# Kernel optimization log

Measured on AMD Instinct MI355X. Metric: run time of the kernel, lower is better.

The kernel has to match this reference:

```python
import jax, jax.numpy as jnp
import numpy as np

IN_C = 256
OUT_C = 256
HID = IN_C * 2
N_POINTS = 262144
N_NODES = 8192
B = 16
MAX_NODES = 512
EPS = 1e-5


def _mlp(h, w1, b1, g1, be1, w2, b2):
    # PyG MLP([C, 2C, out], norm='layer_norm'): lin -> layernorm -> relu -> (dropout, eval=identity) -> lin
    h = h @ w1 + b1
    mu = jnp.mean(h, axis=-1, keepdims=True)
    var = jnp.var(h, axis=-1, keepdims=True)
    h = (h - mu) * jax.lax.rsqrt(var + EPS) * g1 + be1
    h = jax.nn.relu(h)
    return h @ w2 + b2


def setup_inputs() -> dict:
    key = jax.random.key(0)
    ks = jax.random.split(key, 16)
    x = jax.random.normal(ks[0], (N_POINTS, IN_C), dtype=jnp.float32)
    f_point_batches = jnp.sort(jax.random.randint(ks[1], (N_POINTS,), 0, N_NODES)).astype(jnp.int32)
    # equal-sized graphs (16 graphs x 512 nodes), sorted as torch.split/pad_sequence assume
    g_node_batches = jnp.repeat(jnp.arange(B, dtype=jnp.int32), MAX_NODES)
    s = 1.0 / np.sqrt(IN_C)
    s2 = 1.0 / np.sqrt(HID)
    def lin(k, fan_in, shape, scale):
        return jax.random.uniform(k, shape, jnp.float32, -scale, scale)
    params = {}
    for i, name in enumerate(['Wq', 'Wk']):
        base = 2 + i * 6
        params[f'{name}_w1'] = lin(ks[base + 0], IN_C, (IN_C, HID), s)
        params[f'{name}_b1'] = lin(ks[base + 1], IN_C, (HID,), s)
        params[f'{name}_g1'] = jnp.ones((HID,), jnp.float32)
        params[f'{name}_be1'] = jnp.zeros((HID,), jnp.float32)
        params[f'{name}_w2'] = lin(ks[base + 2], HID, (HID, OUT_C), s2)
        params[f'{name}_b2'] = lin(ks[base + 3], HID, (OUT_C,), s2)
    return dict(x=x, f_point_batches=f_point_batches, g_node_batches=g_node_batches,
                num_graphs=B, max_nodes=MAX_NODES, **params)


def reference(x, f_point_batches, g_node_batches, num_graphs, max_nodes,
              Wq_w1, Wq_b1, Wq_g1, Wq_be1, Wq_w2, Wq_b2,
              Wk_w1, Wk_b1, Wk_g1, Wk_be1, Wk_w2, Wk_b2):
    n_nodes = g_node_batches.shape[0]
    C = x.shape[1]
    # scatter_mean over points -> per-node feature means [n_nodes, C]
    sums = jax.ops.segment_sum(x, f_point_batches, num_segments=n_nodes)
    cnt = jax.ops.segment_sum(jnp.ones((x.shape[0],), x.dtype), f_point_batches, num_segments=n_nodes)
    mean = sums / jnp.maximum(cnt, 1.0)[:, None]
    # ragged split by graph + pad_sequence -> [B, max_nodes, C]
    starts = jnp.searchsorted(g_node_batches, jnp.arange(num_graphs, dtype=g_node_batches.dtype))
    pos = jnp.arange(n_nodes) - starts[g_node_batches]
    padded = jnp.zeros((num_graphs, max_nodes, C), x.dtype).at[g_node_batches, pos].set(mean, mode='drop')
    q = _mlp(padded, Wq_w1, Wq_b1, Wq_g1, Wq_be1, Wq_w2, Wq_b2)  # [B, MAXN, out]
    k = _mlp(padded, Wk_w1, Wk_b1, Wk_g1, Wk_be1, Wk_w2, Wk_b2)
    return jnp.einsum('bnd,bmd->bnm', q, k)  # bmm(q, k^T)
```

## Files before the change

### kernel.cpp

```cpp
#include <hip/hip_runtime.h>
#include <hip/hip_bf16.h>

#define N_POINTS 262144
#define N_NODES  8192
#define IN_C     256
#define HID      512
#define OUT_C    256
#define NB       16
#define MAXN     512
#define EPSV     1e-5f

typedef __attribute__((ext_vector_type(8))) short short8;
typedef __attribute__((ext_vector_type(4))) float f32x4;
#define MFMA16(a, b, c) __builtin_amdgcn_mfma_f32_16x16x32_bf16((a), (b), (c), 0, 0, 0)


__global__ __launch_bounds__(256) void prelude_k(
    const int* __restrict__ fpb, int* __restrict__ starts,
    const float* __restrict__ W1q, const float* __restrict__ W1k,
    const float* __restrict__ W2q, const float* __restrict__ W2k,
    __hip_bfloat16* __restrict__ P1q, __hip_bfloat16* __restrict__ P1k,
    __hip_bfloat16* __restrict__ P2q, __hip_bfloat16* __restrict__ P2k)
{
  if (blockIdx.x < 1024) {
    const int i = blockIdx.x * 256 + threadIdx.x;
    const int cur = fpb[i];
    const int prev = (i == 0) ? -1 : fpb[i - 1];
    for (int n = prev + 1; n <= cur; ++n) starts[n] = i;
    if (i == N_POINTS - 1)
      for (int n = cur + 1; n <= N_NODES; ++n) starts[n] = N_POINTS;
    return;
  }
  const int bid = blockIdx.x - 1024;
  const int sel = bid >> 6;
  const float* W; __hip_bfloat16* P; int N;
  switch (sel) {
    case 0:  W = W1q; P = P1q; N = HID;   break;
    case 1:  W = W1k; P = P1k; N = HID;   break;
    case 2:  W = W2q; P = P2q; N = OUT_C; break;
    default: W = W2k; P = P2k; N = OUT_C; break;
  }
  const int idx = (bid & 63) * 256 + threadIdx.x;
  const int NF = N >> 4;
  const int lane = idx & 63;
  const int nf = (idx >> 6) % NF;
  const int ks = idx / (64 * NF);
  const int k0 = ks * 32 + (lane >> 4) * 8;
  const int n  = nf * 16 + (lane & 15);
  __hip_bfloat16 tmp[8];
  #pragma unroll
  for (int j = 0; j < 8; ++j) tmp[j] = __float2bfloat16(W[(size_t)(k0 + j) * N + n]);
  *(uint4*)(P + (size_t)idx * 8) = *(uint4*)tmp;
}

__global__ __launch_bounds__(256) void scatter_mean_k(
    const float* __restrict__ x, const int* __restrict__ starts,
    __hip_bfloat16* __restrict__ mean)
{
  const int node = blockIdx.x;
  const int start = starts[node];
  const int end   = starts[node + 1];
  const int t  = threadIdx.x;
  const int c4 = t & 63;
  const int rr = t >> 6;

  float4 s = make_float4(0.f, 0.f, 0.f, 0.f);
  for (int r = start + rr; r < end; r += 4) {
    float4 v = *(const float4*)(x + (size_t)r * IN_C + c4 * 4);
    s.x += v.x; s.y += v.y; s.z += v.z; s.w += v.w;
  }

  __shared__ float4 red[256];
  red[t] = s;
  __syncthreads();
  if (t < 64) {
    float4 a = red[t], b = red[t + 64], c = red[t + 128], d = red[t + 192];
    const int cnt = end - start;
    const float inv = cnt > 0 ? 1.0f / (float)cnt : 0.0f;
    __hip_bfloat16 o[4];
    o[0] = __float2bfloat16((a.x + b.x + c.x + d.x) * inv);
    o[1] = __float2bfloat16((a.y + b.y + c.y + d.y) * inv);
    o[2] = __float2bfloat16((a.z + b.z + c.z + d.z) * inv);
    o[3] = __float2bfloat16((a.w + b.w + c.w + d.w) * inv);
    *(uint2*)(mean + (size_t)node * IN_C + t * 4) = *(uint2*)o;
  }
}

__global__ __launch_bounds__(256, 2) void mlp_fused_k(
    const __hip_bfloat16* __restrict__ mean,
    const __hip_bfloat16* __restrict__ P1q, const __hip_bfloat16* __restrict__ P2q,
    const float* __restrict__ b1q, const float* __restrict__ g1q,
    const float* __restrict__ be1q, const float* __restrict__ b2q,
    const __hip_bfloat16* __restrict__ P1k, const __hip_bfloat16* __restrict__ P2k,
    const float* __restrict__ b1k, const float* __restrict__ g1k,
    const float* __restrict__ be1k, const float* __restrict__ b2k,
    __hip_bfloat16* __restrict__ qo, __hip_bfloat16* __restrict__ ko)
{
  const int head = blockIdx.y;
  const __hip_bfloat16* P1 = head ? P1k : P1q;
  const __hip_bfloat16* P2 = head ? P2k : P2q;
  const float* b1  = head ? b1k  : b1q;
  const float* g1  = head ? g1k  : g1q;
  const float* be1 = head ? be1k : be1q;
  const float* b2  = head ? b2k  : b2q;
  __hip_bfloat16* out = head ? ko : qo;

  const int row0 = blockIdx.x * 64;
  const int t = threadIdx.x;
  const int w  = t >> 6;
  const int l  = t & 63;
  const int lg = l >> 4;
  const int lm = l & 15;

  __shared__ __hip_bfloat16 HsRaw[64 * 520];
  __shared__ float lnp[4][64][2];
  __hip_bfloat16* As = HsRaw;

  #pragma unroll
  for (int it = 0; it < 8; ++it) {
    const int idx = t + it * 256;
    const int r = idx >> 5, c8 = idx & 31;
    uint4 v = *(const uint4*)(mean + (size_t)(row0 + r) * IN_C + c8 * 8);
    *(uint4*)(As + r * 264 + c8 * 8) = v;
  }
  __syncthreads();

  f32x4 acc1[4][8];
  #pragma unroll
  for (int mi = 0; mi < 4; ++mi)
    #pragma unroll
    for (int nj = 0; nj < 8; ++nj)
      #pragma unroll
      for (int r = 0; r < 4; ++r) acc1[mi][nj][r] = 0.f;

  for (int ks = 0; ks < 8; ++ks) {
    short8 a[4], b[8];
    #pragma unroll
    for (int mi = 0; mi < 4; ++mi)
      a[mi] = *(const short8*)(As + (mi * 16 + lm) * 264 + ks * 32 + lg * 8);
    const __hip_bfloat16* bp = P1 + ((size_t)(ks * 32 + w * 8) * 64 + l) * 8;
    #pragma unroll
    for (int nj = 0; nj < 8; ++nj)
      b[nj] = *(const short8*)(bp + (size_t)nj * 64 * 8);
    #pragma unroll
    for (int mi = 0; mi < 4; ++mi)
      #pragma unroll
      for (int nj = 0; nj < 8; ++nj)
        acc1[mi][nj] = MFMA16(a[mi], b[nj], acc1[mi][nj]);
  }

  float b1v[8], g1v[8], e1v[8];
  #pragma unroll
  for (int nj = 0; nj < 8; ++nj) {
    const int c = w * 128 + nj * 16 + lm;
    b1v[nj] = b1[c]; g1v[nj] = g1[c]; e1v[nj] = be1[c];
  }
  #pragma unroll
  for (int mi = 0; mi < 4; ++mi)
    #pragma unroll
    for (int nj = 0; nj < 8; ++nj)
      #pragma unroll
      for (int r = 0; r < 4; ++r) acc1[mi][nj][r] += b1v[nj];

  float sums[4][4], sqs[4][4];
  #pragma unroll
  for (int mi = 0; mi < 4; ++mi)
    #pragma unroll
    for (int r = 0; r < 4; ++r) {
      float s = 0.f, q = 0.f;
      #pragma unroll
      for (int nj = 0; nj < 8; ++nj) {
        const float xv = acc1[mi][nj][r];
        s += xv; q += xv * xv;
      }
      #pragma unroll
      for (int off = 1; off < 16; off <<= 1) {
        s += __shfl_xor(s, off);
        q += __shfl_xor(q, off);
      }
      sums[mi][r] = s; sqs[mi][r] = q;
    }
  if (lm == 0) {
    #pragma unroll
    for (int mi = 0; mi < 4; ++mi)
      #pragma unroll
      for (int r = 0; r < 4; ++r) {
        const int row = mi * 16 + lg * 4 + r;
        lnp[w][row][0] = sums[mi][r];
        lnp[w][row][1] = sqs[mi][r];
      }
  }
  __syncthreads();

  #pragma unroll
  for (int mi = 0; mi < 4; ++mi) {
    #pragma unroll
    for (int r = 0; r < 4; ++r) {
      const int row = mi * 16 + lg * 4 + r;
      float S = 0.f, Q = 0.f;
      #pragma unroll
      for (int w2 = 0; w2 < 4; ++w2) { S += lnp[w2][row][0]; Q += lnp[w2][row][1]; }
      const float mu = S * (1.0f / HID);
      const float var = Q * (1.0f / HID) - mu * mu;
      const float rs = rsqrtf(var + EPSV);
      #pragma unroll
      for (int nj = 0; nj < 8; ++nj) {
        const float y = (acc1[mi][nj][r] - mu) * rs * g1v[nj] + e1v[nj];
        HsRaw[row * 520 + w * 128 + nj * 16 + lm] = __float2bfloat16(fmaxf(y, 0.f));
      }
    }
  }
  __syncthreads();

  f32x4 acc2[4][4];
  #pragma unroll
  for (int mi = 0; mi < 4; ++mi)
    #pragma unroll
    for (int nj = 0; nj < 4; ++nj)
      #pragma unroll
      for (int r = 0; r < 4; ++r) acc2[mi][nj][r] = 0.f;

  for (int ks = 0; ks < 16; ++ks) {
    short8 a2[4], b2f[4];
    #pragma unroll
    for (int mi = 0; mi < 4; ++mi)
      a2[mi] = *(const short8*)(HsRaw + (mi * 16 + lm) * 520 + ks * 32 + lg * 8);
    const __hip_bfloat16* bp2 = P2 + ((size_t)(ks * 16 + w * 4) * 64 + l) * 8;
    #pragma unroll
    for (int nj = 0; nj < 4; ++nj)
      b2f[nj] = *(const short8*)(bp2 + (size_t)nj * 64 * 8);
    #pragma unroll
    for (int mi = 0; mi < 4; ++mi)
      #pragma unroll
      for (int nj = 0; nj < 4; ++nj)
        acc2[mi][nj] = MFMA16(a2[mi], b2f[nj], acc2[mi][nj]);
  }

  float b2v[4];
  #pragma unroll
  for (int nj = 0; nj < 4; ++nj) b2v[nj] = b2[w * 64 + nj * 16 + lm];
  #pragma unroll
  for (int mi = 0; mi < 4; ++mi)
    #pragma unroll
    for (int nj = 0; nj < 4; ++nj)
      #pragma unroll
      for (int r = 0; r < 4; ++r) {
        const int row = row0 + mi * 16 + lg * 4 + r;
        const int col = w * 64 + nj * 16 + lm;
        out[(size_t)row * OUT_C + col] = __float2bfloat16(acc2[mi][nj][r] + b2v[nj]);
      }
}

__global__ __launch_bounds__(256) void bmm_k(
    const __hip_bfloat16* __restrict__ q, const __hip_bfloat16* __restrict__ k,
    float* __restrict__ out)
{
  const int b  = blockIdx.z;
  const int n0 = blockIdx.x * 128;
  const int m0 = blockIdx.y * 128;
  const int t = threadIdx.x;
  const int w = t >> 6, l = t & 63, lg = l >> 4, lm = l & 15;
  const int wm = w >> 1, wn = w & 1;

  const __hip_bfloat16* qb = q + ((size_t)b * MAXN + n0 + wm * 64) * OUT_C;
  const __hip_bfloat16* kb = k + ((size_t)b * MAXN + m0 + wn * 64) * OUT_C;

  f32x4 acc[4][4];
  #pragma unroll
  for (int mi = 0; mi < 4; ++mi)
    #pragma unroll
    for (int nj = 0; nj < 4; ++nj)
      #pragma unroll
      for (int r = 0; r < 4; ++r) acc[mi][nj][r] = 0.f;

  for (int ks = 0; ks < 8; ++ks) {
    short8 a[4], bb[4];
    #pragma unroll
    for (int mi = 0; mi < 4; ++mi)
      a[mi] = *(const short8*)(qb + (size_t)(mi * 16 + lm) * OUT_C + ks * 32 + lg * 8);
    #pragma unroll
    for (int nj = 0; nj < 4; ++nj)
      bb[nj] = *(const short8*)(kb + (size_t)(nj * 16 + lm) * OUT_C + ks * 32 + lg * 8);
    #pragma unroll
    for (int mi = 0; mi < 4; ++mi)
      #pragma unroll
      for (int nj = 0; nj < 4; ++nj)
        acc[mi][nj] = MFMA16(a[mi], bb[nj], acc[mi][nj]);
  }

  #pragma unroll
  for (int mi = 0; mi < 4; ++mi)
    #pragma unroll
    for (int nj = 0; nj < 4; ++nj)
      #pragma unroll
      for (int r = 0; r < 4; ++r) {
        const int nrow = n0 + wm * 64 + mi * 16 + lg * 4 + r;
        const int mcol = m0 + wn * 64 + nj * 16 + lm;
        out[((size_t)b * MAXN + nrow) * MAXN + mcol] = acc[mi][nj][r];
      }
}

extern "C" void kernel_launch(void* const* d_in, const int* in_sizes, int n_in,
                              void* d_out, int out_size, void* d_ws, size_t ws_size,
                              hipStream_t stream)
{
  const float* x   = (const float*)d_in[0];
  const int*   fpb = (const int*)d_in[1];
  const float* Wq_w1  = (const float*)d_in[5];
  const float* Wq_b1  = (const float*)d_in[6];
  const float* Wq_g1  = (const float*)d_in[7];
  const float* Wq_be1 = (const float*)d_in[8];
  const float* Wq_w2  = (const float*)d_in[9];
  const float* Wq_b2  = (const float*)d_in[10];
  const float* Wk_w1  = (const float*)d_in[11];
  const float* Wk_b1  = (const float*)d_in[12];
  const float* Wk_g1  = (const float*)d_in[13];
  const float* Wk_be1 = (const float*)d_in[14];
  const float* Wk_w2  = (const float*)d_in[15];
  const float* Wk_b2  = (const float*)d_in[16];

  __hip_bfloat16* ws = (__hip_bfloat16*)d_ws;
  __hip_bfloat16* P1q  = ws;
  __hip_bfloat16* P1k  = P1q + 131072;
  __hip_bfloat16* P2q  = P1k + 131072;
  __hip_bfloat16* P2k  = P2q + 131072;
  __hip_bfloat16* mean = P2k + 131072;
  __hip_bfloat16* qo   = mean + 2097152;
  __hip_bfloat16* ko   = qo + 2097152;
  int* starts = (int*)(ko + 2097152);
  float* out = (float*)d_out;

  prelude_k<<<1280, 256, 0, stream>>>(fpb, starts,
      Wq_w1, Wk_w1, Wq_w2, Wk_w2, P1q, P1k, P2q, P2k);
  scatter_mean_k<<<N_NODES, 256, 0, stream>>>(x, starts, mean);
  mlp_fused_k<<<dim3(N_NODES / 64, 2), 256, 0, stream>>>(
      mean, P1q, P2q, Wq_b1, Wq_g1, Wq_be1, Wq_b2,
      P1k, P2k, Wk_b1, Wk_g1, Wk_be1, Wk_b2, qo, ko);
  bmm_k<<<dim3(4, 4, NB), 256, 0, stream>>>(qo, ko, out);
}
```

Before: 102.0 us.

## Retile MLP and BMM kernels for more blocks and add dual accumulators in scatter

The scatter-mean loop now keeps two independent accumulators so more loads are in flight at once. The fused MLP kernel computes both heads in one 512-thread block over 32 rows, giving 256 blocks instead of 256 two-head blocks of 64 rows, and each block stages the shared input only once. The BMM kernel switches to 64x64 tiles (1024 blocks) to fill more compute units. In exchange, each block reuses the weight fragments over fewer rows, so more weight traffic goes to L2.

```diff
diff --git a/kernel.cpp b/kernel.cpp
--- a/kernel.cpp
+++ b/kernel.cpp
@@ -9,6 +9,7 @@
 #define NB       16
 #define MAXN     512
 #define EPSV     1e-5f
+#define NPB      32
 
 typedef __attribute__((ext_vector_type(8))) short short8;
 typedef __attribute__((ext_vector_type(4))) float f32x4;
@@ -64,14 +65,23 @@
   const int c4 = t & 63;
   const int rr = t >> 6;
 
-  float4 s = make_float4(0.f, 0.f, 0.f, 0.f);
-  for (int r = start + rr; r < end; r += 4) {
+  float4 s0 = make_float4(0.f, 0.f, 0.f, 0.f);
+  float4 s1 = make_float4(0.f, 0.f, 0.f, 0.f);
+  int r = start + rr;
+  for (; r + 8 <= end; r += 8) {
+    float4 v0 = *(const float4*)(x + (size_t)r * IN_C + c4 * 4);
+    float4 v1 = *(const float4*)(x + (size_t)(r + 4) * IN_C + c4 * 4);
+    s0.x += v0.x; s0.y += v0.y; s0.z += v0.z; s0.w += v0.w;
+    s1.x += v1.x; s1.y += v1.y; s1.z += v1.z; s1.w += v1.w;
+  }
+  for (; r < end; r += 4) {
     float4 v = *(const float4*)(x + (size_t)r * IN_C + c4 * 4);
-    s.x += v.x; s.y += v.y; s.z += v.z; s.w += v.w;
-  }
+    s0.x += v.x; s0.y += v.y; s0.z += v.z; s0.w += v.w;
+  }
+  s0.x += s1.x; s0.y += s1.y; s0.z += s1.z; s0.w += s1.w;
 
   __shared__ float4 red[256];
-  red[t] = s;
+  red[t] = s0;
   __syncthreads();
   if (t < 64) {
     float4 a = red[t], b = red[t + 64], c = red[t + 128], d = red[t + 192];
@@ -86,7 +96,7 @@
   }
 }
 
-__global__ __launch_bounds__(256, 2) void mlp_fused_k(
+__global__ __launch_bounds__(512, 2) void mlp_fused_k(
     const __hip_bfloat16* __restrict__ mean,
     const __hip_bfloat16* __restrict__ P1q, const __hip_bfloat16* __restrict__ P2q,
     const float* __restrict__ b1q, const float* __restrict__ g1q,
@@ -96,208 +106,181 @@
     const float* __restrict__ be1k, const float* __restrict__ b2k,
     __hip_bfloat16* __restrict__ qo, __hip_bfloat16* __restrict__ ko)
 {
-  const int head = blockIdx.y;
-  const __hip_bfloat16* P1 = head ? P1k : P1q;
-  const __hip_bfloat16* P2 = head ? P2k : P2q;
-  const float* b1  = head ? b1k  : b1q;
-  const float* g1  = head ? g1k  : g1q;
-  const float* be1 = head ? be1k : be1q;
-  const float* b2  = head ? b2k  : b2q;
-  __hip_bfloat16* out = head ? ko : qo;
-
-  const int row0 = blockIdx.x * 64;
+  const int n0 = blockIdx.x * NPB;
   const int t = threadIdx.x;
-  const int w  = t >> 6;
-  const int l  = t & 63;
-  const int lg = l >> 4;
-  const int lm = l & 15;
-
-  __shared__ __hip_bfloat16 HsRaw[64 * 520];
-  __shared__ float lnp[4][64][2];
-  __hip_bfloat16* As = HsRaw;
-
-  #pragma unroll
-  for (int it = 0; it < 8; ++it) {
-    const int idx = t + it * 256;
+  const int w = t >> 6, l = t & 63, lg = l >> 4, lm = l & 15;
+  const int h = w >> 2;
+  const int c = w & 3;
+
+  const __hip_bfloat16* P1 = h ? P1k : P1q;
+  const __hip_bfloat16* P2 = h ? P2k : P2q;
+  const float* b1  = h ? b1k  : b1q;
+  const float* g1  = h ? g1k  : g1q;
+  const float* be1 = h ? be1k : be1q;
+  const float* b2  = h ? b2k  : b2q;
+  __hip_bfloat16* out = h ? ko : qo;
+
+  __shared__ __hip_bfloat16 As[NPB * 264];
+  __shared__ __hip_bfloat16 Hs[2][NPB * 520];
+  __shared__ float lnp[8][NPB][2];
+
+  #pragma unroll
+  for (int it = 0; it < 2; ++it) {
+    const int idx = t + it * 512;
     const int r = idx >> 5, c8 = idx & 31;
-    uint4 v = *(const uint4*)(mean + (size_t)(row0 + r) * IN_C + c8 * 8);
+    uint4 v = *(const uint4*)(mean + (size_t)(n0 + r) * IN_C + c8 * 8);
     *(uint4*)(As + r * 264 + c8 * 8) = v;
   }
   __syncthreads();
 
-  f32x4 acc1[4][8];
-  #pragma unroll
-  for (int mi = 0; mi < 4; ++mi)
+  f32x4 acc1[2][8];
+  #pragma unroll
+  for (int mi = 0; mi < 2; ++mi)
     #pragma unroll
     for (int nj = 0; nj < 8; ++nj)
       #pragma unroll
       for (int r = 0; r < 4; ++r) acc1[mi][nj][r] = 0.f;
 
   for (int ks = 0; ks < 8; ++ks) {
-    short8 a[4], b[8];
-    #pragma unroll
-    for (int mi = 0; mi < 4; ++mi)
-      a[mi] = *(const short8*)(As + (mi * 16 + lm) * 264 + ks * 32 + lg * 8);
-    const __hip_bfloat16* bp = P1 + ((size_t)(ks * 32 + w * 8) * 64 + l) * 8;
+    short8 a0 = *(const short8*)(As + lm * 264 + ks * 32 + lg * 8);
+    short8 a1 = *(const short8*)(As + (16 + lm) * 264 + ks * 32 + lg * 8);
+    const __hip_bfloat16* bp = P1 + ((size_t)(ks * 32 + c * 8) * 64 + l) * 8;
+    #pragma unroll
+    for (int nj = 0; nj < 8; ++nj) {
+      short8 b = *(const short8*)(bp + (size_t)nj * 512);
+      acc1[0][nj] = MFMA16(a0, b, acc1[0][nj]);
+      acc1[1][nj] = MFMA16(a1, b, acc1[1][nj]);
+    }
+  }
+
+  float b1v[8], g1v[8], e1v[8];
+  #pragma unroll
+  for (int nj = 0; nj < 8; ++nj) {
+    const int col = c * 128 + nj * 16 + lm;
+    b1v[nj] = b1[col]; g1v[nj] = g1[col]; e1v[nj] = be1[col];
+  }
+  #pragma unroll
+  for (int mi = 0; mi < 2; ++mi)
     #pragma unroll
     for (int nj = 0; nj < 8; ++nj)
-      b[nj] = *(const short8*)(bp + (size_t)nj * 64 * 8);
-    #pragma unroll
-    for (int mi = 0; mi < 4; ++mi)
-      #pragma unroll
-      for (int nj = 0; nj < 8; ++nj)
-        acc1[mi][nj] = MFMA16(a[mi], b[nj], acc1[mi][nj]);
-  }
-
-  float b1v[8], g1v[8], e1v[8];
-  #pragma unroll
-  for (int nj = 0; nj < 8; ++nj) {
-    const int c = w * 128 + nj * 16 + lm;
-    b1v[nj] = b1[c]; g1v[nj] = g1[c]; e1v[nj] = be1[c];
-  }
-  #pragma unroll
-  for (int mi = 0; mi < 4; ++mi)
-    #pragma unroll
-    for (int nj = 0; nj < 8; ++nj)
       #pragma unroll
       for (int r = 0; r < 4; ++r) acc1[mi][nj][r] += b1v[nj];
 
-  float sums[4][4], sqs[4][4];
-  #pragma unroll
-  for (int mi = 0; mi < 4; ++mi)
+  #pragma unroll
+  for (int mi = 0; mi < 2; ++mi)
     #pragma unroll
     for (int r = 0; r < 4; ++r) {
       float s = 0.f, q = 0.f;
       #pragma unroll
       for (int nj = 0; nj < 8; ++nj) {
-        const float xv = acc1[mi][nj][r];
-        s += xv; q += xv * xv;
+        const float v = acc1[mi][nj][r];
+        s += v; q += v * v;
       }
       #pragma unroll
       for (int off = 1; off < 16; off <<= 1) {
         s += __shfl_xor(s, off);
         q += __shfl_xor(q, off);
       }
-      sums[mi][r] = s; sqs[mi][r] = q;
-    }
-  if (lm == 0) {
-    #pragma unroll
-    for (int mi = 0; mi < 4; ++mi)
-      #pragma unroll
-      for (int r = 0; r < 4; ++r) {
+      if (lm == 0) {
         const int row = mi * 16 + lg * 4 + r;
-        lnp[w][row][0] = sums[mi][r];
-        lnp[w][row][1] = sqs[mi][r];
-      }
-  }
+        lnp[w][row][0] = s;
+        lnp[w][row][1] = q;
+      }
+    }
   __syncthreads();
 
   #pragma unroll
-  for (int mi = 0; mi < 4; ++mi) {
+  for (int mi = 0; mi < 2; ++mi)
     #pragma unroll
     for (int r = 0; r < 4; ++r) {
       const int row = mi * 16 + lg * 4 + r;
       float S = 0.f, Q = 0.f;
       #pragma unroll
-      for (int w2 = 0; w2 < 4; ++w2) { S += lnp[w2][row][0]; Q += lnp[w2][row][1]; }
+      for (int w2 = 0; w2 < 4; ++w2) {
+        S += lnp[h * 4 + w2][row][0];
+        Q += lnp[h * 4 + w2][row][1];
+      }
       const float mu = S * (1.0f / HID);
-      const float var = Q * (1.0f / HID) - mu * mu;
-      const float rs = rsqrtf(var + EPSV);
+      const float rs = rsqrtf(Q * (1.0f / HID) - mu * mu + EPSV);
       #pragma unroll
       for (int nj = 0; nj < 8; ++nj) {
         const float y = (acc1[mi][nj][r] - mu) * rs * g1v[nj] + e1v[nj];
-        HsRaw[row * 520 + w * 128 + nj * 16 + lm] = __float2bfloat16(fmaxf(y, 0.f));
-      }
-    }
-  }
+        Hs[h][row * 520 + c * 128 + nj * 16 + lm] = __float2bfloat16(fmaxf(y, 0.f));
+      }
+    }
   __syncthreads();
 
-  f32x4 acc2[4][4];
-  #pragma unroll
-  for (int mi = 0; mi < 4; ++mi)
+  f32x4 acc2[2][4];
+  #pragma unroll
+  for (int mi = 0; mi < 2; ++mi)
     #pragma unroll
     for (int nj = 0; nj < 4; ++nj)
       #pragma unroll
       for (int r = 0; r < 4; ++r) acc2[mi][nj][r] = 0.f;
 
   for (int ks = 0; ks < 16; ++ks) {
-    short8 a2[4], b2f[4];
-    #pragma unroll
-    for (int mi = 0; mi < 4; ++mi)
-      a2[mi] = *(const short8*)(HsRaw + (mi * 16 + lm) * 520 + ks * 32 + lg * 8);
-    const __hip_bfloat16* bp2 = P2 + ((size_t)(ks * 16 + w * 4) * 64 + l) * 8;
+    short8 a0 = *(const short8*)(Hs[h] + lm * 520 + ks * 32 + lg * 8);
+    short8 a1 = *(const short8*)(Hs[h] + (16 + lm) * 520 + ks * 32 + lg * 8);
+    const __hip_bfloat16* bp = P2 + ((size_t)(ks * 16 + c * 4) * 64 + l) * 8;
+    #pragma unroll
+    for (int nj = 0; nj < 4; ++nj) {
+      short8 b = *(const short8*)(bp + (size_t)nj * 512);
+      acc2[0][nj] = MFMA16(a0, b, acc2[0][nj]);
+      acc2[1][nj] = MFMA16(a1, b, acc2[1][nj]);
+    }
+  }
+
+  float b2v[4];
+  #pragma unroll
+  for (int nj = 0; nj < 4; ++nj) b2v[nj] = b2[c * 64 + nj * 16 + lm];
+  #pragma unroll
+  for (int mi = 0; mi < 2; ++mi)
     #pragma unroll
     for (int nj = 0; nj < 4; ++nj)
-      b2f[nj] = *(const short8*)(bp2 + (size_t)nj * 64 * 8);
-    #pragma unroll
-    for (int mi = 0; mi < 4; ++mi)
-      #pragma unroll
-      for (int nj = 0; nj < 4; ++nj)
-        acc2[mi][nj] = MFMA16(a2[mi], b2f[nj], acc2[mi][nj]);
-  }
-
-  float b2v[4];
-  #pragma unroll
-  for (int nj = 0; nj < 4; ++nj) b2v[nj] = b2[w * 64 + nj * 16 + lm];
-  #pragma unroll
-  for (int mi = 0; mi < 4; ++mi)
-    #pragma unroll
-    for (int nj = 0; nj < 4; ++nj)
       #pragma unroll
       for (int r = 0; r < 4; ++r) {
-        const int row = row0 + mi * 16 + lg * 4 + r;
-        const int col = w * 64 + nj * 16 + lm;
+        const int row = n0 + mi * 16 + lg * 4 + r;
+        const int col = c * 64 + nj * 16 + lm;
         out[(size_t)row * OUT_C + col] = __float2bfloat16(acc2[mi][nj][r] + b2v[nj]);
       }
 }
 
-__global__ __launch_bounds__(256) void bmm_k(
+__global__ __launch_bounds__(256, 4) void bmm_k(
     const __hip_bfloat16* __restrict__ q, const __hip_bfloat16* __restrict__ k,
     float* __restrict__ out)
 {
   const int b  = blockIdx.z;
-  const int n0 = blockIdx.x * 128;
-  const int m0 = blockIdx.y * 128;
+  const int n0 = blockIdx.x * 64;
+  const int m0 = blockIdx.y * 64;
   const int t = threadIdx.x;
   const int w = t >> 6, l = t & 63, lg = l >> 4, lm = l & 15;
-  const int wm = w >> 1, wn = w & 1;
-
-  const __hip_bfloat16* qb = q + ((size_t)b * MAXN + n0 + wm * 64) * OUT_C;
-  const __hip_bfloat16* kb = k + ((size_t)b * MAXN + m0 + wn * 64) * OUT_C;
-
-  f32x4 acc[4][4];
-  #pragma unroll
-  for (int mi = 0; mi < 4; ++mi)
-    #pragma unroll
-    for (int nj = 0; nj < 4; ++nj)
-      #pragma unroll
-      for (int r = 0; r < 4; ++r) acc[mi][nj][r] = 0.f;
+
+  const __hip_bfloat16* qb = q + ((size_t)b * MAXN + n0 + w * 16) * OUT_C;
+  const __hip_bfloat16* kb = k + ((size_t)b * MAXN + m0) * OUT_C;
+
+  f32x4 acc[4];
+  #pragma unroll
+  for (int nj = 0; nj < 4; ++nj)
+    #pragma unroll
+    for (int r = 0; r < 4; ++r) acc[nj][r] = 0.f;
 
   for (int ks = 0; ks < 8; ++ks) {
-    short8 a[4], bb[4];
-    #pragma unroll
-    for (int mi = 0; mi < 4; ++mi)
-      a[mi] = *(const short8*)(qb + (size_t)(mi * 16 + lm) * OUT_C + ks * 32 + lg * 8);
-    #pragma unroll
-    for (int nj = 0; nj < 4; ++nj)
-      bb[nj] = *(const short8*)(kb + (size_t)(nj * 16 + lm) * OUT_C + ks * 32 + lg * 8);
-    #pragma unroll
-    for (int mi = 0; mi < 4; ++mi)
-      #pragma unroll
-      for (int nj = 0; nj < 4; ++nj)
-        acc[mi][nj] = MFMA16(a[mi], bb[nj], acc[mi][nj]);
-  }
-
-  #pragma unroll
-  for (int mi = 0; mi < 4; ++mi)
-    #pragma unroll
-    for (int nj = 0; nj < 4; ++nj)
-      #pragma unroll
-      for (int r = 0; r < 4; ++r) {
-        const int nrow = n0 + wm * 64 + mi * 16 + lg * 4 + r;
-        const int mcol = m0 + wn * 64 + nj * 16 + lm;
-        out[((size_t)b * MAXN + nrow) * MAXN + mcol] = acc[mi][nj][r];
-      }
+    short8 a = *(const short8*)(qb + (size_t)lm * OUT_C + ks * 32 + lg * 8);
+    #pragma unroll
+    for (int nj = 0; nj < 4; ++nj) {
+      short8 bb = *(const short8*)(kb + (size_t)(nj * 16 + lm) * OUT_C + ks * 32 + lg * 8);
+      acc[nj] = MFMA16(a, bb, acc[nj]);
+    }
+  }
+
+  #pragma unroll
+  for (int nj = 0; nj < 4; ++nj)
+    #pragma unroll
+    for (int r = 0; r < 4; ++r) {
+      const int nrow = n0 + w * 16 + lg * 4 + r;
+      const int mcol = m0 + nj * 16 + lm;
+      out[((size_t)b * MAXN + nrow) * MAXN + mcol] = acc[nj][r];
+    }
 }
 
 extern "C" void kernel_launch(void* const* d_in, const int* in_sizes, int n_in,
@@ -333,8 +316,8 @@
   prelude_k<<<1280, 256, 0, stream>>>(fpb, starts,
       Wq_w1, Wk_w1, Wq_w2, Wk_w2, P1q, P1k, P2q, P2k);
   scatter_mean_k<<<N_NODES, 256, 0, stream>>>(x, starts, mean);
-  mlp_fused_k<<<dim3(N_NODES / 64, 2), 256, 0, stream>>>(
+  mlp_fused_k<<<N_NODES / NPB, 512, 0, stream>>>(
       mean, P1q, P2q, Wq_b1, Wq_g1, Wq_be1, Wq_b2,
       P1k, P2k, Wk_b1, Wk_g1, Wk_be1, Wk_b2, qo, ko);
-  bmm_k<<<dim3(4, 4, NB), 256, 0, stream>>>(qo, ko, out);
-}
+  bmm_k<<<dim3(8, 8, NB), 256, 0, stream>>>(qo, ko, out);
+}
```

After: 95.51 us. -6.3%, faster.
